# Optimization experiments

Hardware: AMD Instinct MI355X
Metric: run time of the kernel (lower is better)

## Reference

```python
import jax, jax.numpy as jnp
import numpy as np

PLP_ORDER = 16
N_CHANNEL = 40
FFT_LENGTH = 512
SAMPLE_RATE = 16000
LIFTER = 22
COMP_FACTOR = 0.33
FLOOR = 1e-5
F_MIN = 0.0
F_MAX = SAMPLE_RATE / 2


def _hz_to_mel(hz):
    return 1127.0 * np.log1p(np.asarray(hz, dtype=np.float64) / 700.0)


def _mel_to_hz(mel):
    return 700.0 * np.expm1(np.asarray(mel, dtype=np.float64) / 1127.0)


def _build_constants():
    # SPTK-style mel filter bank (triangular in mel domain).
    mel_min = _hz_to_mel(F_MIN)
    mel_max = _hz_to_mel(F_MAX)
    lower_bin = max(1, int(F_MIN / SAMPLE_RATE * FFT_LENGTH + 1.5))
    upper_bin = min(FFT_LENGTH // 2, int(F_MAX / SAMPLE_RATE * FFT_LENGTH + 0.5))
    seed = np.arange(1, N_CHANNEL + 2)
    cf_mel = (mel_max - mel_min) / (N_CHANNEL + 1) * seed + mel_min  # (C+1,)
    bins = np.arange(lower_bin, upper_bin)
    mel = _hz_to_mel(SAMPLE_RATE * bins / FFT_LENGTH)
    ch = np.searchsorted(cf_mel, mel, side='left')  # first center freq >= mel
    diff = cf_mel - np.concatenate([[mel_min], cf_mel[:-1]])
    w = (cf_mel[ch] - mel) / diff[ch]
    H = np.zeros((len(bins), N_CHANNEL))
    rows = np.arange(len(bins))
    low = ch - 1
    m_lo = low >= 0
    H[rows[m_lo], low[m_lo]] += w[m_lo]
    m_hi = ch <= N_CHANNEL - 1
    H[rows[m_hi], ch[m_hi]] += 1.0 - w[m_hi]
    # Equal-loudness curve over the first C center frequencies (in Hz).
    cf_hz = _mel_to_hz(cf_mel)
    f2 = cf_hz[:N_CHANNEL] ** 2
    eql = (f2 / (f2 + 160000.0)) ** 2 * (f2 + 1440000.0) / (f2 + 9610000.0)
    # Liftering vector, v[0] = 2.
    m = np.arange(PLP_ORDER + 1)
    lift = 1.0 + LIFTER / 2.0 * np.sin(np.pi / LIFTER * m)
    lift[0] = 2.0
    return lower_bin, upper_bin, H.astype(np.float32), eql.astype(np.float32), lift.astype(np.float32)


LOWER_BIN, UPPER_BIN, H_NP, EQL_NP, LIFT_NP = _build_constants()


def _levinson_durbin(r):
    # r: (..., M+1) autocorrelation -> (gain K, LPC coefficients a_1..a_M)
    M = PLP_ORDER
    E = r[..., 0]
    a = jnp.zeros(r.shape[:-1] + (M,), r.dtype)
    for i in range(1, M + 1):
        acc = r[..., i]
        if i > 1:
            acc = acc + jnp.einsum('...j,...j->...', a[..., : i - 1], r[..., 1:i][..., ::-1])
        k = -acc / E
        if i > 1:
            a = a.at[..., : i - 1].set(a[..., : i - 1] + k[..., None] * a[..., : i - 1][..., ::-1])
        a = a.at[..., i - 1].set(k)
        E = E * (1.0 - k * k)
    return jnp.sqrt(E), a


def _lpc_to_cepstrum(K, a):
    # c0 = log K; c_m = -a_m - sum_{k=1}^{m-1} (k/m) c_k a_{m-k}
    M = PLP_ORDER
    c = [jnp.log(K)]
    for m in range(1, M + 1):
        acc = a[..., m - 1]
        for k in range(1, m):
            acc = acc + (k / m) * c[k] * a[..., m - k - 1]
        c.append(-acc)
    return jnp.stack(c, axis=-1)  # (..., M+1)


def _plp(x):
    H = jnp.asarray(H_NP)
    eql = jnp.asarray(EQL_NP)
    lift = jnp.asarray(LIFT_NP)
    # Mel filter bank on power spectrum (use_power=True)
    fb = jnp.matmul(x[..., LOWER_BIN:UPPER_BIN], H)          # (..., C)
    logfb = jnp.log(jnp.maximum(fb, FLOOR))
    # Equal-loudness scaling + cubic-root amplitude compression
    y = (jnp.exp(logfb) * eql) ** COMP_FACTOR                # (..., C)
    # replicate1: duplicate first and last channels
    y = jnp.concatenate([y[..., :1], y, y[..., -1:]], axis=-1)  # (..., C+2)
    n = y.shape[-1]
    # hfft with norm='forward' -> inverse-FFT-like autocorrelation
    r = jnp.fft.hfft(y) / (2 * (n - 1))
    r = r[..., : PLP_ORDER + 1]
    K, a = _levinson_durbin(r)
    c = _lpc_to_cepstrum(K, a)
    c = c * lift
    return c[..., 1:]  # out_format 'y': PLP without C0, (..., M)


def setup_inputs() -> dict:
    key = jax.random.key(0)
    x = jax.random.uniform(key, (32, 4096, FFT_LENGTH // 2 + 1), dtype=jnp.float32)
    return {"x": x}


def reference(x):
    return _plp(x)
```

## Files before the change

### kernel.cpp

```cpp
#include <hip/hip_runtime.h>

#define NCH   40
#define MORD  16
#define NR    17
#define NY    42
#define NBINS 257
#define FPB   64

namespace cfg {

constexpr double PI  = 3.14159265358979323846264338327950288;
constexpr double LN2 = 0.693147180559945309417232121458176568;

constexpr double cexp(double x) {
    double t = 1.0, s = 1.0;
    for (int i = 1; i < 40; ++i) { t *= x / i; s += t; }
    return s;
}

constexpr double clog(double z) {
    double lg = 0.0;
    while (z > 1.4142135623730951) { z *= 0.5; lg += LN2; }
    while (z < 0.7071067811865476) { z *= 2.0; lg -= LN2; }
    double u = (z - 1.0) / (z + 1.0), u2 = u * u, t = u, s = u;
    for (int k = 1; k < 24; ++k) { t *= u2; s += t / (2.0 * k + 1.0); }
    return lg + 2.0 * s;
}

constexpr double ccos(double x) {
    double tp = 2.0 * PI;
    double q = x / tp;
    long long k = (long long)(q + (q >= 0.0 ? 0.5 : -0.5));
    double r = x - (double)k * tp;
    double r2 = r * r, t = 1.0, s = 1.0;
    for (int i = 1; i < 20; ++i) { t *= -r2 / ((2.0 * i - 1.0) * (2.0 * i)); s += t; }
    return s;
}

constexpr double csin(double x) { return ccos(x - PI / 2.0); }

struct Tab {
    int   start[43];
    float w[257];
    float eql[NCH];
    float lift[NR];
    float ct[NR][NY];
    constexpr Tab() : start(), w(), eql(), lift(), ct() {
        const double lmax  = clog(87.0 / 7.0);
        const double U1127 = lmax / 41.0;
        for (int c = 0; c <= 41; ++c) {
            double thr = 22.4 * (cexp((double)c * U1127) - 1.0);
            int s = (int)thr + 1;
            if (s < 1) s = 1;
            if (s > 256) s = 256;
            start[c] = s;
        }
        start[42 - 1] = start[41];
        for (int c = 0; c <= 40; ++c) {
            for (int b = start[c]; b < start[c + 1]; ++b) {
                double mel = 1127.0 * clog(1.0 + (double)b * 31.25 / 700.0);
                double t   = mel / (1127.0 * U1127);
                w[b] = (float)(t - (double)c);
            }
        }
        for (int c = 0; c < NCH; ++c) {
            double cf = 700.0 * (cexp((double)(c + 1) * U1127) - 1.0);
            double f2 = cf * cf;
            double e  = f2 / (f2 + 160000.0);
            e = e * e * (f2 + 1440000.0) / (f2 + 9610000.0);
            eql[c] = (float)e;
        }
        for (int m = 0; m < NR; ++m)
            lift[m] = (float)(1.0 + 11.0 * csin(PI * (double)m / 22.0));
        lift[0] = 2.0f;
        for (int l = 0; l < NR; ++l)
            for (int j = 0; j < NY; ++j) {
                double s = (j == 0 || j == NY - 1) ? 1.0 : 2.0;
                ct[l][j] = (float)(s * ccos(PI * (double)(j * l) / 41.0) / 82.0);
            }
    }
};

constexpr Tab T{};

}

__global__ __launch_bounds__(FPB) void plp_kernel(const float* __restrict__ x,
                                                  float* __restrict__ out,
                                                  int nframes)
{
    using cfg::T;
    __shared__ float slab[FPB * NBINS];
    const int tid = threadIdx.x;
    const long long F0 = (long long)blockIdx.x * FPB;

    {
        const float* base = x + F0 * NBINS + tid * 4;
        const float* gend = x + (long long)nframes * NBINS;
        #pragma unroll
        for (int k = 0; k < 65; ++k) {
            const int off = (k < 64) ? k * 256 : (FPB * NBINS - 256);
            const float* src = base + off;
            if (src + 4 > gend) src = gend - 4;
            __builtin_amdgcn_global_load_lds(
                (const __attribute__((address_space(1))) void*)src,
                (__attribute__((address_space(3))) void*)(slab + off),
                16, 0, 0);
        }
    }
    __syncthreads();

    const long long frame = F0 + tid;
    if (frame >= nframes) return;
    const float* __restrict__ fr = slab + tid * NBINS;

    float fb[NCH];
    #pragma unroll
    for (int c = 0; c < NCH; ++c) fb[c] = 0.f;

    #pragma unroll
    for (int c = 0; c <= 40; ++c) {
        #pragma unroll
        for (int b = T.start[c]; b < T.start[c + 1]; ++b) {
            float xv = fr[b];
            const float wa = T.w[b];
            if (c < 40) fb[c]     = fmaf(wa, xv, fb[c]);
            if (c >= 1) fb[c - 1] = fmaf(1.0f - wa, xv, fb[c - 1]);
        }
    }

    float ys[NY];
    #pragma unroll
    for (int c = 0; c < NCH; ++c) {
        float v = fmaxf(fb[c], 1e-5f) * T.eql[c];
        ys[c + 1] = __expf(0.33f * __logf(v));
    }
    ys[0] = ys[1];
    ys[NY - 1] = ys[NY - 2];

    float r[NR];
    #pragma unroll
    for (int l = 0; l < NR; ++l) {
        float acc = 0.f;
        #pragma unroll
        for (int j = 0; j < NY; ++j) acc = fmaf(T.ct[l][j], ys[j], acc);
        r[l] = acc;
    }

    float a[MORD];
    #pragma unroll
    for (int i = 0; i < MORD; ++i) a[i] = 0.f;
    float E = r[0];
    #pragma unroll
    for (int i = 1; i <= MORD; ++i) {
        float acc = r[i];
        #pragma unroll
        for (int j = 0; j < i - 1; ++j) acc = fmaf(a[j], r[i - 1 - j], acc);
        float k = -acc / E;
        const int half = (i - 1) / 2;
        #pragma unroll
        for (int j = 0; j < half; ++j) {
            float t1 = a[j], t2 = a[i - 2 - j];
            a[j]         = fmaf(k, t2, t1);
            a[i - 2 - j] = fmaf(k, t1, t2);
        }
        if ((i - 1) & 1) a[half] = fmaf(k, a[half], a[half]);
        a[i - 1] = k;
        E = E * (1.f - k * k);
    }

    float cc[NR];
    #pragma unroll
    for (int m = 1; m <= MORD; ++m) {
        float acc = a[m - 1];
        #pragma unroll
        for (int k2 = 1; k2 < m; ++k2)
            acc = fmaf(((float)k2 / (float)m) * cc[k2], a[m - k2 - 1], acc);
        cc[m] = -acc;
    }

    float o[16];
    #pragma unroll
    for (int m = 1; m <= MORD; ++m) o[m - 1] = cc[m] * T.lift[m];

    float4* op = reinterpret_cast<float4*>(out + (size_t)frame * 16);
    op[0] = make_float4(o[0],  o[1],  o[2],  o[3]);
    op[1] = make_float4(o[4],  o[5],  o[6],  o[7]);
    op[2] = make_float4(o[8],  o[9],  o[10], o[11]);
    op[3] = make_float4(o[12], o[13], o[14], o[15]);
}

extern "C" void kernel_launch(void* const* d_in, const int* in_sizes, int n_in,
                              void* d_out, int out_size, void* d_ws, size_t ws_size,
                              hipStream_t stream) {
    const float* x   = (const float*)d_in[0];
    float*      outp = (float*)d_out;
    int nframes = in_sizes[0] / NBINS;
    int nblocks = (nframes + FPB - 1) / FPB;
    plp_kernel<<<nblocks, FPB, 0, stream>>>(x, outp, nframes);
}
```

Baseline: 204.6 us.

## Stage spectra as fp16 in LDS, loop filterbank, fold cosine transform by symmetry

The input slab is now loaded with plain float4 loads and stored in LDS as half precision instead of using direct global-to-LDS loads. The filterbank becomes a rolled loop over segments that computes each channel from a weighted sum and a plain sum, with weights staged in LDS. The cosine autocorrelation is folded using even/odd symmetry, and intermediates pass through LDS in rolled loops. Levinson division is replaced by a hardware reciprocal and the cepstrum recursion drops per-term divisions. These changes cut register pressure and LDS footprint to raise occupancy, at the cost of fp16 rounding of inputs and extra LDS traffic.

After: 250.5 us. 22.5% more time.

```diff
diff --git a/kernel.cpp b/kernel.cpp
--- a/kernel.cpp
+++ b/kernel.cpp
@@ -1,4 +1,5 @@
 #include <hip/hip_runtime.h>
+#include <hip/hip_fp16.h>
 
 #define NCH   40
 #define MORD  16
@@ -6,6 +7,8 @@
 #define NY    42
 #define NBINS 257
 #define FPB   64
+#define SLABF (FPB * NBINS)
+#define YSTR  43
 
 namespace cfg {
 
@@ -44,8 +47,8 @@
     float w[257];
     float eql[NCH];
     float lift[NR];
-    float ct[NR][NY];
-    constexpr Tab() : start(), w(), eql(), lift(), ct() {
+    float ctf[NR][21];
+    constexpr Tab() : start(), w(), eql(), lift(), ctf() {
         const double lmax  = clog(87.0 / 7.0);
         const double U1127 = lmax / 41.0;
         for (int c = 0; c <= 41; ++c) {
@@ -55,7 +58,7 @@
             if (s > 256) s = 256;
             start[c] = s;
         }
-        start[42 - 1] = start[41];
+        start[42] = start[41];
         for (int c = 0; c <= 40; ++c) {
             for (int b = start[c]; b < start[c + 1]; ++b) {
                 double mel = 1127.0 * clog(1.0 + (double)b * 31.25 / 700.0);
@@ -74,14 +77,14 @@
             lift[m] = (float)(1.0 + 11.0 * csin(PI * (double)m / 22.0));
         lift[0] = 2.0f;
         for (int l = 0; l < NR; ++l)
-            for (int j = 0; j < NY; ++j) {
-                double s = (j == 0 || j == NY - 1) ? 1.0 : 2.0;
-                ct[l][j] = (float)(s * ccos(PI * (double)(j * l) / 41.0) / 82.0);
+            for (int j = 0; j <= 20; ++j) {
+                double s = (j == 0) ? 1.0 : 2.0;
+                ctf[l][j] = (float)(s * ccos(PI * (double)(j * l) / 41.0) / 82.0);
             }
     }
 };
 
-constexpr Tab T{};
+__device__ constexpr Tab T{};
 
 }
 
@@ -90,62 +93,93 @@
                                                   int nframes)
 {
     using cfg::T;
-    __shared__ float slab[FPB * NBINS];
+    __shared__ __half slab[SLABF];
+    __shared__ float  wlds[NBINS];
+    __shared__ float  ysl[FPB * YSTR];
     const int tid = threadIdx.x;
     const long long F0 = (long long)blockIdx.x * FPB;
 
+    for (int i = tid; i < NBINS; i += FPB) wlds[i] = T.w[i];
+
     {
-        const float* base = x + F0 * NBINS + tid * 4;
-        const float* gend = x + (long long)nframes * NBINS;
-        #pragma unroll
-        for (int k = 0; k < 65; ++k) {
-            const int off = (k < 64) ? k * 256 : (FPB * NBINS - 256);
-            const float* src = base + off;
-            if (src + 4 > gend) src = gend - 4;
-            __builtin_amdgcn_global_load_lds(
-                (const __attribute__((address_space(1))) void*)src,
-                (__attribute__((address_space(3))) void*)(slab + off),
-                16, 0, 0);
+        const float4* gsrc = reinterpret_cast<const float4*>(x + F0 * NBINS);
+        const long long maxq = ((long long)nframes * NBINS) / 4 - (F0 * NBINS) / 4;
+        #pragma unroll 16
+        for (int k = 0; k < 64; ++k) {
+            long long i  = (long long)k * 64 + tid;
+            long long ii = (i < maxq) ? i : (maxq - 1);
+            float4 g = gsrc[ii];
+            __half2 h0 = __halves2half2(__float2half_rn(g.x), __float2half_rn(g.y));
+            __half2 h1 = __halves2half2(__float2half_rn(g.z), __float2half_rn(g.w));
+            *reinterpret_cast<__half2*>(&slab[i * 4])     = h0;
+            *reinterpret_cast<__half2*>(&slab[i * 4 + 2]) = h1;
+        }
+        if (tid < 16) {
+            long long i  = 4096 + tid;
+            long long ii = (i < maxq) ? i : (maxq - 1);
+            float4 g = gsrc[ii];
+            __half2 h0 = __halves2half2(__float2half_rn(g.x), __float2half_rn(g.y));
+            __half2 h1 = __halves2half2(__float2half_rn(g.z), __float2half_rn(g.w));
+            *reinterpret_cast<__half2*>(&slab[i * 4])     = h0;
+            *reinterpret_cast<__half2*>(&slab[i * 4 + 2]) = h1;
         }
     }
     __syncthreads();
 
     const long long frame = F0 + tid;
     if (frame >= nframes) return;
-    const float* __restrict__ fr = slab + tid * NBINS;
-
-    float fb[NCH];
-    #pragma unroll
-    for (int c = 0; c < NCH; ++c) fb[c] = 0.f;
-
-    #pragma unroll
-    for (int c = 0; c <= 40; ++c) {
-        #pragma unroll
-        for (int b = T.start[c]; b < T.start[c + 1]; ++b) {
-            float xv = fr[b];
-            const float wa = T.w[b];
-            if (c < 40) fb[c]     = fmaf(wa, xv, fb[c]);
-            if (c >= 1) fb[c - 1] = fmaf(1.0f - wa, xv, fb[c - 1]);
-        }
-    }
-
-    float ys[NY];
-    #pragma unroll
-    for (int c = 0; c < NCH; ++c) {
-        float v = fmaxf(fb[c], 1e-5f) * T.eql[c];
-        ys[c + 1] = __expf(0.33f * __logf(v));
-    }
-    ys[0] = ys[1];
-    ys[NY - 1] = ys[NY - 2];
-
-    float r[NR];
-    #pragma unroll
+    const __half* fr = slab + tid * NBINS;
+
+    float prevWA = 0.f;
+    #pragma unroll 1
+    for (int s = 0; s <= 40; ++s) {
+        const int b0 = T.start[s];
+        const int b1 = T.start[s + 1];
+        float WA = 0.f, SX = 0.f;
+        #pragma unroll 4
+        for (int b = b0; b < b1; ++b) {
+            float xv = __half2float(fr[b]);
+            float wv = wlds[b];
+            WA = fmaf(wv, xv, WA);
+            SX += xv;
+        }
+        if (s >= 1) {
+            float fbv = prevWA + (SX - WA);
+            float v   = fmaxf(fbv, 1e-5f) * T.eql[s - 1];
+            ysl[tid * YSTR + (s - 1)] = __expf(0.33f * __logf(v));
+        }
+        prevWA = WA;
+    }
+
+    float ye[21], yo[21];
+    {
+        float yv[40];
+        #pragma unroll
+        for (int c = 0; c < 40; ++c) yv[c] = ysl[tid * YSTR + c];
+        ye[0] = yv[0] + yv[39];  yo[0] = yv[0] - yv[39];
+        #pragma unroll
+        for (int j = 1; j <= 20; ++j) {
+            float aa = yv[j - 1], bb = yv[40 - j];
+            ye[j] = aa + bb;  yo[j] = aa - bb;
+        }
+    }
+
+    #pragma unroll 1
     for (int l = 0; l < NR; ++l) {
         float acc = 0.f;
-        #pragma unroll
-        for (int j = 0; j < NY; ++j) acc = fmaf(T.ct[l][j], ys[j], acc);
-        r[l] = acc;
-    }
+        if (l & 1) {
+            #pragma unroll
+            for (int j = 0; j <= 20; ++j) acc = fmaf(T.ctf[l][j], yo[j], acc);
+        } else {
+            #pragma unroll
+            for (int j = 0; j <= 20; ++j) acc = fmaf(T.ctf[l][j], ye[j], acc);
+        }
+        ysl[tid * YSTR + l] = acc;
+    }
+
+    float r[NR];
+    #pragma unroll
+    for (int l = 0; l < NR; ++l) r[l] = ysl[tid * YSTR + l];
 
     float a[MORD];
     #pragma unroll
@@ -156,7 +190,7 @@
         float acc = r[i];
         #pragma unroll
         for (int j = 0; j < i - 1; ++j) acc = fmaf(a[j], r[i - 1 - j], acc);
-        float k = -acc / E;
+        float k = -acc * __builtin_amdgcn_rcpf(E);
         const int half = (i - 1) / 2;
         #pragma unroll
         for (int j = 0; j < half; ++j) {
@@ -169,14 +203,16 @@
         E = E * (1.f - k * k);
     }
 
-    float cc[NR];
+    float cc[NR], ccs[NR];
     #pragma unroll
     for (int m = 1; m <= MORD; ++m) {
-        float acc = a[m - 1];
+        float acc = 0.f;
         #pragma unroll
         for (int k2 = 1; k2 < m; ++k2)
-            acc = fmaf(((float)k2 / (float)m) * cc[k2], a[m - k2 - 1], acc);
-        cc[m] = -acc;
+            acc = fmaf(ccs[k2], a[m - k2 - 1], acc);
+        float cm = -(a[m - 1] + acc * (1.0f / (float)m));
+        cc[m]  = cm;
+        ccs[m] = (float)m * cm;
     }
 
     float o[16];
```
